# Kernel optimization log

Hardware: AMD Instinct MI355X
Metric: run time of the kernel (lower is better)

Reference implementation:

```python
import jax, jax.numpy as jnp
import numpy as np

B, S, D, H = 4, 2048, 1024, 16
DK = D // H
SCALE = 1.0 / np.float32(np.sqrt(DK))


def setup_inputs() -> dict:
    key = jax.random.key(0)
    ks = jax.random.split(key, 11)
    w = lambda k: (jax.random.normal(k, (D, D), jnp.float32) * 0.02)
    b = lambda k: (jax.random.normal(k, (D,), jnp.float32) * 0.02)
    return {
        "Q": jax.random.normal(ks[0], (B, S, D), jnp.float32),
        "K": jax.random.normal(ks[1], (B, S, D), jnp.float32),
        "V": jax.random.normal(ks[2], (B, S, D), jnp.float32),
        "Wq": w(ks[3]), "bq": b(ks[4]),
        "Wk": w(ks[5]), "bk": b(ks[6]),
        "Wv": w(ks[7]), "bv": b(ks[8]),
        "Wo": w(ks[9]), "bo": b(ks[10]),
        # causal mask, broadcast over batch and heads: [1,1,S,S]
        "mask": jnp.tril(jnp.ones((1, 1, S, S), dtype=bool)),
    }


def reference(Q, K, V, Wq, bq, Wk, bk, Wv, bv, Wo, bo, mask):
    def proj(x, W, bias):
        # [B,S,D] -> [B,H,S,DK]
        return (x @ W + bias).reshape(B, S, H, DK).transpose(0, 2, 1, 3)

    q = proj(Q, Wq, bq)
    k = proj(K, Wk, bk)
    v = proj(V, Wv, bv)
    scores = jnp.einsum("bhqd,bhkd->bhqk", q, k) * SCALE  # [B,H,S,S]
    scores = jnp.where(mask, scores, jnp.float32(-1e9))
    attn = jax.nn.softmax(scores, axis=-1)
    out = jnp.einsum("bhqk,bhkd->bhqd", attn, v)  # [B,H,S,DK]
    out = out.transpose(0, 2, 1, 3).reshape(B, S, D)
    return out @ Wo + bo
```

## Files before the change

kernel.cpp:

```cpp
#include <hip/hip_runtime.h>
#include <hip/hip_bf16.h>
#include <stdint.h>

#define BB 4
#define SS 2048
#define DD 1024
#define HH 16
#define DKK 64
#define MM (BB * SS)

typedef __hip_bfloat16 bf16;
typedef __attribute__((ext_vector_type(8))) short frag8;
typedef __attribute__((ext_vector_type(4))) float f32x4;

#define GLDS16(g, l)                                                        \
  __builtin_amdgcn_global_load_lds(                                         \
      (const __attribute__((address_space(1))) void*)(g),                   \
      (__attribute__((address_space(3))) void*)(l), 16, 0, 0)

#define MFMA __builtin_amdgcn_mfma_f32_16x16x32_bf16

__device__ __forceinline__ unsigned short f2bu(float f) {
  __hip_bfloat16 h = __float2bfloat16(f);
  return *reinterpret_cast<unsigned short*>(&h);
}

struct WtArgs {
  const float* s[3];
  unsigned short* d[3];
};
__global__ __launch_bounds__(256) void wtrans_kernel(WtArgs a) {
  const float* __restrict__ W = a.s[blockIdx.z];
  unsigned short* __restrict__ Wt = a.d[blockIdx.z];
  __shared__ float t[64][68];
  const int n0 = blockIdx.x * 64, k0 = blockIdx.y * 64;
  const int tid = threadIdx.x;
#pragma unroll
  for (int it = 0; it < 4; ++it) {
    const int kk = it * 16 + (tid >> 4);
    const int nn = (tid & 15) * 4;
    const float4 v = *(const float4*)&W[(size_t)(k0 + kk) * DD + n0 + nn];
    *(float4*)&t[kk][nn] = v;
  }
  __syncthreads();
#pragma unroll
  for (int it = 0; it < 2; ++it) {
    const int n = it * 32 + (tid >> 3);
    const int c = tid & 7;
    frag8 pk;
#pragma unroll
    for (int j = 0; j < 8; ++j) pk[j] = (short)f2bu(t[c * 8 + j][n]);
    *(frag8*)&Wt[(size_t)(n0 + n) * DD + k0 + c * 8] = pk;
  }
}

struct CvtArgs {
  const float* s[3];
  unsigned short* d[3];
};
__global__ __launch_bounds__(256) void cvt_kernel(CvtArgs a) {
  const float* __restrict__ src = a.s[blockIdx.y];
  unsigned short* __restrict__ dst = a.d[blockIdx.y];
  const size_t i = ((size_t)blockIdx.x * 256 + threadIdx.x) * 8;
  const float4 v0 = *(const float4*)&src[i];
  const float4 v1 = *(const float4*)&src[i + 4];
  frag8 pk;
  pk[0] = (short)f2bu(v0.x); pk[1] = (short)f2bu(v0.y);
  pk[2] = (short)f2bu(v0.z); pk[3] = (short)f2bu(v0.w);
  pk[4] = (short)f2bu(v1.x); pk[5] = (short)f2bu(v1.y);
  pk[6] = (short)f2bu(v1.z); pk[7] = (short)f2bu(v1.w);
  *(frag8*)&dst[i] = pk;
}

struct GArgs {
  const void* A[3];
  const unsigned short* W[3];
  const float* bias[3];
  void* out[3];
  float oscale[3];
  int abf16[3];
  int omode[3];
};
__global__ __launch_bounds__(256) void gemm_kernel(GArgs ga) {
  constexpr int K = DD;
  const int z = blockIdx.z;
  const void* __restrict__ Av = ga.A[z];
  const unsigned short* __restrict__ Wt = ga.W[z];
  const float* __restrict__ bias = ga.bias[z];
  void* __restrict__ outv = ga.out[z];
  const float oscale = ga.oscale[z];
  const int abf = ga.abf16[z];
  const int omode = ga.omode[z];

  __shared__ unsigned short Bs[2][128 * 64];
  __shared__ unsigned short As[2][128 * 64];
  const int tid = threadIdx.x;
  const int wave = tid >> 6, lane = tid & 63, quad = lane >> 4, l15 = lane & 15;
  const int wr = wave >> 1, wc = wave & 1;
  const int mt = blockIdx.x * 8 + (blockIdx.y >> 3);
  const int nt = blockIdx.y & 7;
  const int m0 = mt * 128, n0 = nt * 128;

  f32x4 acc[4][4] = {};
  float4 r0[4], r1[4];

  auto stageB = [&](int buf, int k0) {
#pragma unroll
    for (int c = 0; c < 4; ++c) {
      const int row = c * 32 + wave * 8 + (lane >> 3);
      const int gc = ((lane & 7) ^ (row & 7)) * 8;
      const unsigned short* g = &Wt[(size_t)(n0 + row) * K + k0 + gc];
      unsigned off = __builtin_amdgcn_readfirstlane(
          (unsigned)(buf * 16384 + (c * 32 + wave * 8) * 128));
      GLDS16(g, (char*)&Bs[0][0] + off);
    }
  };
  auto stageA16 = [&](int buf, int k0) {
    const unsigned short* A = (const unsigned short*)Av;
#pragma unroll
    for (int c = 0; c < 4; ++c) {
      const int row = c * 32 + wave * 8 + (lane >> 3);
      const int gc = ((lane & 7) ^ (row & 7)) * 8;
      const unsigned short* g = &A[(size_t)(m0 + row) * K + k0 + gc];
      unsigned off = __builtin_amdgcn_readfirstlane(
          (unsigned)(buf * 16384 + (c * 32 + wave * 8) * 128));
      GLDS16(g, (char*)&As[0][0] + off);
    }
  };
  auto loadA32 = [&](int k0) {
    const float* A = (const float*)Av;
#pragma unroll
    for (int it = 0; it < 4; ++it) {
      const int row = it * 32 + (tid >> 3);
      const int c = tid & 7;
      r0[it] = *(const float4*)&A[(size_t)(m0 + row) * K + k0 + c * 8];
      r1[it] = *(const float4*)&A[(size_t)(m0 + row) * K + k0 + c * 8 + 4];
    }
  };
  auto writeA32 = [&](int buf) {
#pragma unroll
    for (int it = 0; it < 4; ++it) {
      const int row = it * 32 + (tid >> 3);
      const int c = tid & 7;
      frag8 pk;
      pk[0] = (short)f2bu(r0[it].x); pk[1] = (short)f2bu(r0[it].y);
      pk[2] = (short)f2bu(r0[it].z); pk[3] = (short)f2bu(r0[it].w);
      pk[4] = (short)f2bu(r1[it].x); pk[5] = (short)f2bu(r1[it].y);
      pk[6] = (short)f2bu(r1[it].z); pk[7] = (short)f2bu(r1[it].w);
      *(frag8*)&As[buf][row * 64 + ((c ^ (row & 7)) * 8)] = pk;
    }
  };
  auto compute = [&](int buf) {
#pragma unroll
    for (int s = 0; s < 2; ++s) {
      frag8 af[4], bfr[4];
#pragma unroll
      for (int mi = 0; mi < 4; ++mi)
        af[mi] = *(const frag8*)&As[buf][(wr * 64 + mi * 16 + l15) * 64 +
                                         (((s * 4 + quad) ^ (l15 & 7)) * 8)];
#pragma unroll
      for (int ni = 0; ni < 4; ++ni)
        bfr[ni] = *(const frag8*)&Bs[buf][(wc * 64 + ni * 16 + l15) * 64 +
                                          (((s * 4 + quad) ^ (l15 & 7)) * 8)];
#pragma unroll
      for (int mi = 0; mi < 4; ++mi)
#pragma unroll
        for (int ni = 0; ni < 4; ++ni)
          acc[mi][ni] = MFMA(af[mi], bfr[ni], acc[mi][ni], 0, 0, 0);
    }
  };

  if (abf) {
    stageB(0, 0);
    stageA16(0, 0);
  } else {
    loadA32(0);
    stageB(0, 0);
    writeA32(0);
  }
  __syncthreads();

#pragma unroll 1
  for (int t = 0; t < 16; t += 2) {
    if (t + 1 < 16) {
      if (abf) {
        stageB(1, (t + 1) * 64);
        stageA16(1, (t + 1) * 64);
      } else {
        loadA32((t + 1) * 64);
        stageB(1, (t + 1) * 64);
      }
    }
    compute(0);
    if (!abf && t + 1 < 16) writeA32(1);
    __syncthreads();
    if (t + 2 < 16) {
      if (abf) {
        stageB(0, (t + 2) * 64);
        stageA16(0, (t + 2) * 64);
      } else {
        loadA32((t + 2) * 64);
        stageB(0, (t + 2) * 64);
      }
    }
    compute(1);
    if (!abf && t + 2 < 16) writeA32(0);
    __syncthreads();
  }

#pragma unroll
  for (int mi = 0; mi < 4; ++mi) {
#pragma unroll
    for (int ni = 0; ni < 4; ++ni) {
#pragma unroll
      for (int r = 0; r < 4; ++r) {
        const int grow = m0 + wr * 64 + mi * 16 + quad * 4 + r;
        const int gcol = n0 + wc * 64 + ni * 16 + l15;
        const float val = (acc[mi][ni][r] + bias[gcol]) * oscale;
        if (omode == 2) {
          ((float*)outv)[(size_t)grow * DD + gcol] = val;
        } else {
          const int b = grow / SS, s = grow % SS;
          const int h = gcol / DKK, dk = gcol % DKK;
          unsigned short* o = (unsigned short*)outv;
          if (omode == 0)
            o[(((size_t)(b * HH + h)) * SS + s) * DKK + dk] = f2bu(val);
          else
            o[(((size_t)(b * HH + h)) * DKK + dk) * SS + s] = f2bu(val);
        }
      }
    }
  }
}

__global__ __launch_bounds__(256) void fattn_kernel(
    const unsigned short* __restrict__ q, const unsigned short* __restrict__ k,
    const unsigned short* __restrict__ vt, unsigned short* __restrict__ ctx) {
  __shared__ unsigned short Ks[2][64 * 64];
  __shared__ unsigned short Vs[2][64 * 64];
  __shared__ unsigned short P_lds[4][16][36];
  const int tid = threadIdx.x;
  const int wave = tid >> 6, lane = tid & 63, quad = lane >> 4, l15 = lane & 15;
  const int bh = blockIdx.x & 63;
  const int tp = blockIdx.x >> 6;
  const size_t qkb = (size_t)bh * SS * DKK;
  const size_t vtb = (size_t)bh * DKK * SS;
  const int b = bh / HH, h = bh % HH;

  frag8 ones;
#pragma unroll
  for (int s = 0; s < 8; ++s) ones[s] = (short)0x3F80;

  auto stage = [&](int buf, int jt) {
#pragma unroll
    for (int c = 0; c < 2; ++c) {
      const int row = wave * 16 + c * 8 + (lane >> 3);
      const int gc = ((lane & 7) ^ (row & 7)) * 8;
      const unsigned short* g = &k[qkb + (size_t)(jt * 64 + row) * DKK + gc];
      unsigned off = __builtin_amdgcn_readfirstlane(
          (unsigned)(buf * 8192 + (wave * 16 + c * 8) * 128));
      GLDS16(g, (char*)&Ks[0][0] + off);
    }
#pragma unroll
    for (int c = 0; c < 2; ++c) {
      const int row = wave * 16 + c * 8 + (lane >> 3);
      const int gc = ((lane & 7) ^ (row & 7)) * 8;
      const unsigned short* g = &vt[vtb + (size_t)row * SS + jt * 64 + gc];
      unsigned off = __builtin_amdgcn_readfirstlane(
          (unsigned)(buf * 8192 + (wave * 16 + c * 8) * 128));
      GLDS16(g, (char*)&Vs[0][0] + off);
    }
  };

  for (int half = 0; half < 2; ++half) {
    const int t = half ? (31 - tp) : tp;
    const int q0 = t * 64 + wave * 16;

    const frag8 aq0 =
        *(const frag8*)&q[qkb + (size_t)(q0 + l15) * DKK + quad * 8];
    const frag8 aq1 =
        *(const frag8*)&q[qkb + (size_t)(q0 + l15) * DKK + 32 + quad * 8];

    f32x4 oacc[4] = {};
    f32x4 lacc = {};

    const int nT = t + 1;
    stage(0, 0);
    __syncthreads();

    for (int jt = 0; jt < nT; ++jt) {
      const int p = jt & 1;
      if (jt + 1 < nT) stage(1 - p, jt + 1);
      const bool diag = (jt == t);

#pragma unroll
      for (int jsub = 0; jsub < 2; ++jsub) {
        f32x4 sc[2];
#pragma unroll
        for (int g = 0; g < 2; ++g) {
          const int row = jsub * 32 + g * 16 + l15;
          const frag8 kf0 =
              *(const frag8*)&Ks[p][row * 64 + ((quad ^ (l15 & 7)) * 8)];
          const frag8 kf1 =
              *(const frag8*)&Ks[p][row * 64 + (((4 + quad) ^ (l15 & 7)) * 8)];
          f32x4 z = {};
          z = MFMA(aq0, kf0, z, 0, 0, 0);
          sc[g] = MFMA(aq1, kf1, z, 0, 0, 0);
        }
        float p0[4], p1[4];
        if (diag) {
          const int jg = jt * 64 + jsub * 32;
#pragma unroll
          for (int r = 0; r < 4; ++r) {
            const int ig = q0 + quad * 4 + r;
            p0[r] = (jg + l15 <= ig) ? __expf(sc[0][r]) : 0.f;
            p1[r] = (jg + 16 + l15 <= ig) ? __expf(sc[1][r]) : 0.f;
          }
        } else {
#pragma unroll
          for (int r = 0; r < 4; ++r) {
            p0[r] = __expf(sc[0][r]);
            p1[r] = __expf(sc[1][r]);
          }
        }
#pragma unroll
        for (int r = 0; r < 4; ++r) {
          P_lds[wave][quad * 4 + r][l15] = f2bu(p0[r]);
          P_lds[wave][quad * 4 + r][16 + l15] = f2bu(p1[r]);
        }
        const frag8 pa = *(const frag8*)&P_lds[wave][l15][quad * 8];
#pragma unroll
        for (int c = 0; c < 4; ++c) {
          const int vrow = c * 16 + l15;
          const int chunk = ((jsub * 4 + quad) ^ (l15 & 7));
          const frag8 vf = *(const frag8*)&Vs[p][vrow * 64 + chunk * 8];
          oacc[c] = MFMA(pa, vf, oacc[c], 0, 0, 0);
        }
        lacc = MFMA(pa, ones, lacc, 0, 0, 0);
      }
      __syncthreads();
    }

#pragma unroll
    for (int r = 0; r < 4; ++r) {
      const float inv = 1.f / lacc[r];
      const int ig = q0 + quad * 4 + r;
#pragma unroll
      for (int c = 0; c < 4; ++c)
        ctx[((size_t)(b * SS + ig)) * DD + h * DKK + c * 16 + l15] =
            f2bu(oacc[c][r] * inv);
    }
  }
}

extern "C" void kernel_launch(void* const* d_in, const int* in_sizes, int n_in,
                              void* d_out, int out_size, void* d_ws,
                              size_t ws_size, hipStream_t stream) {
  const float* Q = (const float*)d_in[0];
  const float* K = (const float*)d_in[1];
  const float* V = (const float*)d_in[2];
  const float* Wq = (const float*)d_in[3];
  const float* bq = (const float*)d_in[4];
  const float* Wk = (const float*)d_in[5];
  const float* bk = (const float*)d_in[6];
  const float* Wv = (const float*)d_in[7];
  const float* bv = (const float*)d_in[8];
  const float* Wo = (const float*)d_in[9];
  const float* bo = (const float*)d_in[10];

  const size_t NE = (size_t)MM * DD;
  unsigned short* ctx = (unsigned short*)d_ws;
  unsigned short* qp = ctx + NE;
  unsigned short* kp = qp + NE;
  unsigned short* vtp = kp + NE;
  unsigned short* Qb = vtp + NE;
  unsigned short* Kb = Qb + NE;
  unsigned short* Vb = Kb + NE;
  unsigned short* Wqt = ctx;
  unsigned short* Wkt = ctx + 1048576;
  unsigned short* Wvt = ctx + 2097152;
  unsigned short* Wot = qp;

  const bool fastQK = ws_size >= (size_t)6 * NE * sizeof(unsigned short);
  const bool fastV = ws_size >= (size_t)7 * NE * sizeof(unsigned short);

  const dim3 gg(8, 64, 3);

  WtArgs wa1;
  wa1.s[0] = Wq; wa1.s[1] = Wk; wa1.s[2] = Wv;
  wa1.d[0] = Wqt; wa1.d[1] = Wkt; wa1.d[2] = Wvt;
  wtrans_kernel<<<dim3(16, 16, 3), 256, 0, stream>>>(wa1);

  int ncvt = 0;
  CvtArgs ca;
  if (fastQK) {
    ca.s[0] = Q; ca.d[0] = Qb;
    ca.s[1] = K; ca.d[1] = Kb;
    ncvt = 2;
    if (fastV) { ca.s[2] = V; ca.d[2] = Vb; ncvt = 3; }
    cvt_kernel<<<dim3(NE / 2048, ncvt), 256, 0, stream>>>(ca);
  }

  GArgs g3;
  g3.A[0] = fastQK ? (const void*)Qb : (const void*)Q;
  g3.A[1] = fastQK ? (const void*)Kb : (const void*)K;
  g3.A[2] = fastV ? (const void*)Vb : (const void*)V;
  g3.W[0] = Wqt; g3.W[1] = Wkt; g3.W[2] = Wvt;
  g3.bias[0] = bq; g3.bias[1] = bk; g3.bias[2] = bv;
  g3.out[0] = qp; g3.out[1] = kp; g3.out[2] = vtp;
  g3.oscale[0] = 0.125f; g3.oscale[1] = 1.f; g3.oscale[2] = 1.f;
  g3.abf16[0] = fastQK ? 1 : 0; g3.abf16[1] = fastQK ? 1 : 0;
  g3.abf16[2] = fastV ? 1 : 0;
  g3.omode[0] = 0; g3.omode[1] = 0; g3.omode[2] = 1;
  gemm_kernel<<<gg, 256, 0, stream>>>(g3);

  fattn_kernel<<<dim3(BB * HH * 16), 256, 0, stream>>>(qp, kp, vtp, ctx);

  WtArgs wa2;
  wa2.s[0] = Wo; wa2.d[0] = Wot;
  wa2.s[1] = Wo; wa2.d[1] = Wot;
  wa2.s[2] = Wo; wa2.d[2] = Wot;
  wtrans_kernel<<<dim3(16, 16, 1), 256, 0, stream>>>(wa2);

  GArgs go;
  go.A[0] = (const void*)ctx; go.W[0] = Wot; go.bias[0] = bo;
  go.out[0] = (void*)d_out; go.oscale[0] = 1.f;
  go.abf16[0] = 1; go.omode[0] = 2;
  go.A[1] = go.A[0]; go.W[1] = go.W[0]; go.bias[1] = go.bias[0];
  go.out[1] = go.out[0]; go.oscale[1] = 1.f; go.abf16[1] = 1; go.omode[1] = 2;
  go.A[2] = go.A[0]; go.W[2] = go.W[0]; go.bias[2] = go.bias[0];
  go.out[2] = go.out[0]; go.oscale[2] = 1.f; go.abf16[2] = 1; go.omode[2] = 2;
  gemm_kernel<<<dim3(8, 64, 1), 256, 0, stream>>>(go);
}
```

Baseline: 361.9 us.

## Add 256x256-tile 8-wave GEMM with split-phase LDS pipelining for projections

Adds a new GEMM kernel using 256x256 output tiles, 512 threads (8 waves), and a four-quadrant MFMA schedule. Global-to-LDS prefetch of the next K-slice is interleaved between compute phases, with explicit barriers and raised wave priority around the MFMA runs. Workgroup IDs are remapped across the 8 XCDs. It is used for both the QKV and output projections when the workspace allows bf16 inputs. Larger tiles raise data reuse and cut global traffic, at the cost of fewer workgroups (384 and 128) and higher register and LDS pressure.

```diff
diff --git a/kernel.cpp b/kernel.cpp
--- a/kernel.cpp
+++ b/kernel.cpp
@@ -19,6 +19,8 @@
       (__attribute__((address_space(3))) void*)(l), 16, 0, 0)
 
 #define MFMA __builtin_amdgcn_mfma_f32_16x16x32_bf16
+#define SBAR asm volatile("s_barrier" ::: "memory")
+#define WAITV0 asm volatile("s_waitcnt vmcnt(0)" ::: "memory")
 
 __device__ __forceinline__ unsigned short f2bu(float f) {
   __hip_bfloat16 h = __float2bfloat16(f);
@@ -81,6 +83,142 @@
   int abf16[3];
   int omode[3];
 };
+
+__global__ __launch_bounds__(512, 2) void gemm8_kernel(GArgs ga) {
+  constexpr int K = DD;
+  const int nwg = gridDim.x;
+  const int q = nwg >> 3;
+  const int o = blockIdx.x;
+  const int wgid = (o & 7) * q + (o >> 3);
+  const int z = wgid >> 7;
+  const int rem = wgid & 127;
+  const int mt = rem >> 2, nt = rem & 3;
+  const int m0 = mt * 256, n0 = nt * 256;
+
+  const unsigned short* __restrict__ A = (const unsigned short*)ga.A[z];
+  const unsigned short* __restrict__ Wt = ga.W[z];
+  const float* __restrict__ bias = ga.bias[z];
+  void* __restrict__ outv = ga.out[z];
+  const float oscale = ga.oscale[z];
+  const int omode = ga.omode[z];
+
+  __shared__ unsigned short As[2][256 * 64];
+  __shared__ unsigned short Bs[2][256 * 64];
+
+  const int tid = threadIdx.x;
+  const int wave = tid >> 6, lane = tid & 63, quad = lane >> 4, l15 = lane & 15;
+  const int wr = wave >> 2, wc = wave & 3;
+
+  f32x4 acc[8][4] = {};
+  frag8 af[4][2], bfv[2][2];
+
+  auto stage4 = [&](int b, int k0, int half) {
+#pragma unroll
+    for (int ii = 0; ii < 4; ++ii) {
+      const int i = half * 4 + ii;
+      const int g = i * 8 + wave;
+      const int rs = (g & 31) * 8;
+      const int lrow = rs + (lane >> 3);
+      const int gc = ((lane & 7) ^ (lane >> 3)) * 8;
+      const unsigned off = __builtin_amdgcn_readfirstlane(
+          (unsigned)(b * 32768 + rs * 128));
+      if (g < 32) {
+        GLDS16(&A[(size_t)(m0 + lrow) * K + k0 + gc], (char*)&As[0][0] + off);
+      } else {
+        GLDS16(&Wt[(size_t)(n0 + lrow) * K + k0 + gc], (char*)&Bs[0][0] + off);
+      }
+    }
+  };
+  auto rdA = [&](int bt, int mh) {
+#pragma unroll
+    for (int mi = 0; mi < 4; ++mi)
+#pragma unroll
+      for (int s = 0; s < 2; ++s)
+        af[mi][s] = *(const frag8*)&As[bt][(wr * 128 + mh * 64 + mi * 16 + l15) *
+                                              64 +
+                                          (((s * 4 + quad) ^ (l15 & 7)) * 8)];
+  };
+  auto rdB = [&](int bt, int nh) {
+#pragma unroll
+    for (int ni = 0; ni < 2; ++ni)
+#pragma unroll
+      for (int s = 0; s < 2; ++s)
+        bfv[ni][s] = *(const frag8*)&Bs[bt][(wc * 64 + nh * 32 + ni * 16 + l15) *
+                                                64 +
+                                            (((s * 4 + quad) ^ (l15 & 7)) * 8)];
+  };
+  auto mma = [&](int mh, int nh) {
+    __builtin_amdgcn_s_setprio(1);
+#pragma unroll
+    for (int s = 0; s < 2; ++s)
+#pragma unroll
+      for (int mi = 0; mi < 4; ++mi)
+#pragma unroll
+        for (int ni = 0; ni < 2; ++ni)
+          acc[mh * 4 + mi][nh * 2 + ni] = MFMA(
+              af[mi][s], bfv[ni][s], acc[mh * 4 + mi][nh * 2 + ni], 0, 0, 0);
+    __builtin_amdgcn_s_setprio(0);
+  };
+
+  stage4(0, 0, 0);
+  stage4(0, 0, 1);
+  WAITV0;
+  __syncthreads();
+
+#pragma unroll 1
+  for (int t = 0; t < 16; ++t) {
+    const int bt = t & 1;
+    const int nb = bt ^ 1;
+    const bool pf = (t + 1 < 16);
+    const int k1 = (t + 1) * 64;
+    if (pf) stage4(nb, k1, 0);
+    rdA(bt, 0);
+    rdB(bt, 0);
+    SBAR;
+    mma(0, 0);
+    SBAR;
+    if (pf) stage4(nb, k1, 1);
+    rdB(bt, 1);
+    SBAR;
+    mma(0, 1);
+    SBAR;
+    rdA(bt, 1);
+    rdB(bt, 0);
+    SBAR;
+    mma(1, 0);
+    SBAR;
+    rdB(bt, 1);
+    SBAR;
+    mma(1, 1);
+    WAITV0;
+    SBAR;
+  }
+
+#pragma unroll
+  for (int mi = 0; mi < 8; ++mi) {
+#pragma unroll
+    for (int ni = 0; ni < 4; ++ni) {
+#pragma unroll
+      for (int r = 0; r < 4; ++r) {
+        const int grow = m0 + wr * 128 + mi * 16 + quad * 4 + r;
+        const int gcol = n0 + wc * 64 + ni * 16 + l15;
+        const float val = (acc[mi][ni][r] + bias[gcol]) * oscale;
+        if (omode == 2) {
+          ((float*)outv)[(size_t)grow * DD + gcol] = val;
+        } else {
+          const int b = grow / SS, s = grow % SS;
+          const int h = gcol / DKK, dk = gcol % DKK;
+          unsigned short* outp = (unsigned short*)outv;
+          if (omode == 0)
+            outp[(((size_t)(b * HH + h)) * SS + s) * DKK + dk] = f2bu(val);
+          else
+            outp[(((size_t)(b * HH + h)) * DKK + dk) * SS + s] = f2bu(val);
+        }
+      }
+    }
+  }
+}
+
 __global__ __launch_bounds__(256) void gemm_kernel(GArgs ga) {
   constexpr int K = DD;
   const int z = blockIdx.z;
@@ -116,25 +254,25 @@
     }
   };
   auto stageA16 = [&](int buf, int k0) {
-    const unsigned short* A = (const unsigned short*)Av;
+    const unsigned short* Ap = (const unsigned short*)Av;
 #pragma unroll
     for (int c = 0; c < 4; ++c) {
       const int row = c * 32 + wave * 8 + (lane >> 3);
       const int gc = ((lane & 7) ^ (row & 7)) * 8;
-      const unsigned short* g = &A[(size_t)(m0 + row) * K + k0 + gc];
+      const unsigned short* g = &Ap[(size_t)(m0 + row) * K + k0 + gc];
       unsigned off = __builtin_amdgcn_readfirstlane(
           (unsigned)(buf * 16384 + (c * 32 + wave * 8) * 128));
       GLDS16(g, (char*)&As[0][0] + off);
     }
   };
   auto loadA32 = [&](int k0) {
-    const float* A = (const float*)Av;
+    const float* Ap = (const float*)Av;
 #pragma unroll
     for (int it = 0; it < 4; ++it) {
       const int row = it * 32 + (tid >> 3);
       const int c = tid & 7;
-      r0[it] = *(const float4*)&A[(size_t)(m0 + row) * K + k0 + c * 8];
-      r1[it] = *(const float4*)&A[(size_t)(m0 + row) * K + k0 + c * 8 + 4];
+      r0[it] = *(const float4*)&Ap[(size_t)(m0 + row) * K + k0 + c * 8];
+      r1[it] = *(const float4*)&Ap[(size_t)(m0 + row) * K + k0 + c * 8 + 4];
     }
   };
   auto writeA32 = [&](int buf) {
@@ -153,20 +291,20 @@
   auto compute = [&](int buf) {
 #pragma unroll
     for (int s = 0; s < 2; ++s) {
-      frag8 af[4], bfr[4];
+      frag8 a2[4], b2[4];
 #pragma unroll
       for (int mi = 0; mi < 4; ++mi)
-        af[mi] = *(const frag8*)&As[buf][(wr * 64 + mi * 16 + l15) * 64 +
+        a2[mi] = *(const frag8*)&As[buf][(wr * 64 + mi * 16 + l15) * 64 +
                                          (((s * 4 + quad) ^ (l15 & 7)) * 8)];
 #pragma unroll
       for (int ni = 0; ni < 4; ++ni)
-        bfr[ni] = *(const frag8*)&Bs[buf][(wc * 64 + ni * 16 + l15) * 64 +
-                                          (((s * 4 + quad) ^ (l15 & 7)) * 8)];
+        b2[ni] = *(const frag8*)&Bs[buf][(wc * 64 + ni * 16 + l15) * 64 +
+                                         (((s * 4 + quad) ^ (l15 & 7)) * 8)];
 #pragma unroll
       for (int mi = 0; mi < 4; ++mi)
 #pragma unroll
         for (int ni = 0; ni < 4; ++ni)
-          acc[mi][ni] = MFMA(af[mi], bfr[ni], acc[mi][ni], 0, 0, 0);
+          acc[mi][ni] = MFMA(a2[mi], b2[ni], acc[mi][ni], 0, 0, 0);
     }
   };
 
@@ -222,11 +360,11 @@
         } else {
           const int b = grow / SS, s = grow % SS;
           const int h = gcol / DKK, dk = gcol % DKK;
-          unsigned short* o = (unsigned short*)outv;
+          unsigned short* outp = (unsigned short*)outv;
           if (omode == 0)
-            o[(((size_t)(b * HH + h)) * SS + s) * DKK + dk] = f2bu(val);
+            outp[(((size_t)(b * HH + h)) * SS + s) * DKK + dk] = f2bu(val);
           else
-            o[(((size_t)(b * HH + h)) * DKK + dk) * SS + s] = f2bu(val);
+            outp[(((size_t)(b * HH + h)) * DKK + dk) * SS + s] = f2bu(val);
         }
       }
     }
@@ -384,19 +522,16 @@
   const bool fastQK = ws_size >= (size_t)6 * NE * sizeof(unsigned short);
   const bool fastV = ws_size >= (size_t)7 * NE * sizeof(unsigned short);
 
-  const dim3 gg(8, 64, 3);
-
   WtArgs wa1;
   wa1.s[0] = Wq; wa1.s[1] = Wk; wa1.s[2] = Wv;
   wa1.d[0] = Wqt; wa1.d[1] = Wkt; wa1.d[2] = Wvt;
   wtrans_kernel<<<dim3(16, 16, 3), 256, 0, stream>>>(wa1);
 
-  int ncvt = 0;
   CvtArgs ca;
   if (fastQK) {
+    int ncvt = 2;
     ca.s[0] = Q; ca.d[0] = Qb;
     ca.s[1] = K; ca.d[1] = Kb;
-    ncvt = 2;
     if (fastV) { ca.s[2] = V; ca.d[2] = Vb; ncvt = 3; }
     cvt_kernel<<<dim3(NE / 2048, ncvt), 256, 0, stream>>>(ca);
   }
@@ -412,7 +547,11 @@
   g3.abf16[0] = fastQK ? 1 : 0; g3.abf16[1] = fastQK ? 1 : 0;
   g3.abf16[2] = fastV ? 1 : 0;
   g3.omode[0] = 0; g3.omode[1] = 0; g3.omode[2] = 1;
-  gemm_kernel<<<gg, 256, 0, stream>>>(g3);
+  if (fastV) {
+    gemm8_kernel<<<dim3(384), 512, 0, stream>>>(g3);
+  } else {
+    gemm_kernel<<<dim3(8, 64, 3), 256, 0, stream>>>(g3);
+  }
 
   fattn_kernel<<<dim3(BB * HH * 16), 256, 0, stream>>>(qp, kp, vtp, ctx);
 
@@ -430,5 +569,9 @@
   go.out[1] = go.out[0]; go.oscale[1] = 1.f; go.abf16[1] = 1; go.omode[1] = 2;
   go.A[2] = go.A[0]; go.W[2] = go.W[0]; go.bias[2] = go.bias[0];
   go.out[2] = go.out[0]; go.oscale[2] = 1.f; go.abf16[2] = 1; go.omode[2] = 2;
-  gemm_kernel<<<dim3(8, 64, 1), 256, 0, stream>>>(go);
-}
+  if (fastV) {
+    gemm8_kernel<<<dim3(128), 512, 0, stream>>>(go);
+  } else {
+    gemm_kernel<<<dim3(8, 64, 1), 256, 0, stream>>>(go);
+  }
+}
```

After: 433.0 us. 19.6% more time.
